# Optimization experiments

Hardware: AMD Instinct MI355X
Metric: run time of the kernel (lower is better)

Reference implementation:

```python
import jax, jax.numpy as jnp
import numpy as np

HEADS = 8
DIM_HEAD = 64
SCALE = DIM_HEAD ** -0.5
POS_DIM = 64


def _sincos_pe(H, W, dim, dtype):
    # matches build_2d_sincos_pos_embed: [1, dim, H, W]
    y = jnp.linspace(-1.0, 1.0, H)[:, None] * jnp.ones((1, W), jnp.float32)
    x = jnp.ones((H, 1), jnp.float32) * jnp.linspace(-1.0, 1.0, W)[None, :]
    omega = 1.0 / (10000.0 ** (jnp.arange(dim // 4, dtype=jnp.float32) / (dim // 4)))
    px = x[..., None] * omega  # [H, W, dim//4]
    py = y[..., None] * omega
    pe = jnp.concatenate([jnp.sin(px), jnp.cos(px), jnp.sin(py), jnp.cos(py)], axis=-1)
    return pe.transpose(2, 0, 1)[None].astype(dtype)


def _conv2d(x, w):
    return jax.lax.conv_general_dilated(
        x, w, (1, 1), 'SAME', dimension_numbers=('NCHW', 'OIHW', 'NCHW'))


def _sobel(d):
    kx = jnp.array([[1, 0, -1], [2, 0, -2], [1, 0, -1]], jnp.float32).reshape(1, 1, 3, 3)
    ky = jnp.array([[1, 2, 1], [0, 0, 0], [-1, -2, -1]], jnp.float32).reshape(1, 1, 3, 3)
    return _conv2d(d, kx), _conv2d(d, ky)


def setup_inputs() -> dict:
    key = jax.random.key(0)
    ks = jax.random.split(key, 8)
    B, C, H, W = 2, 256, 64, 64
    hid = HEADS * DIM_HEAD  # 512
    s = 0.02
    return {
        'x': jax.random.normal(ks[0], (B, C, H, W), jnp.float32),
        'dsm': jax.random.uniform(ks[1], (B, 1, H, W), jnp.float32),
        'wq': jax.random.normal(ks[2], (hid, C), jnp.float32) * s,
        'wkv': jax.random.normal(ks[3], (2 * hid, C + 1), jnp.float32) * s,
        'wout': jax.random.normal(ks[4], (C, hid), jnp.float32) * s,
        'bout': jnp.zeros((C,), jnp.float32),
        'w_hape': jax.random.normal(ks[5], (hid, POS_DIM + 3), jnp.float32) * s,
        'b_hape': jnp.zeros((hid,), jnp.float32),
        'w_alpha': jax.random.normal(ks[6], (1, 1, 3, 3), jnp.float32) * 0.1,
        'b_alpha': jnp.zeros((1,), jnp.float32),
    }


def reference(x, dsm, wq, wkv, wout, bout, w_hape, b_hape, w_alpha, b_alpha):
    B, C, H, W = x.shape
    hid = wq.shape[0]
    # per-sample min-max normalize DSM over spatial dims
    dmin = dsm.min(axis=(2, 3), keepdims=True)
    dmax = dsm.max(axis=(2, 3), keepdims=True)
    d = (dsm - dmin) / (dmax - dmin + 1e-6)
    # HAPE: [PE | h | grad_h] -> 1x1 conv to hidden
    pe = jnp.broadcast_to(_sincos_pe(H, W, POS_DIM, x.dtype), (B, POS_DIM, H, W))
    gx, gy = _sobel(d)
    hape_in = jnp.concatenate([pe, d, gx, gy], axis=1)  # [B, 67, H, W]
    hape_k = jnp.einsum('oc,bchw->bohw', w_hape, hape_in) + b_hape[None, :, None, None]
    # QKV via 1x1 convs
    q = jnp.einsum('oc,bchw->bohw', wq, x)
    kv = jnp.einsum('oc,bchw->bohw', wkv, jnp.concatenate([x, d], axis=1))
    k = kv[:, :hid] + hape_k
    v = kv[:, hid:]
    to_heads = lambda t: t.reshape(B, HEADS, DIM_HEAD, H * W)  # b (h c) x y -> b h c (xy)
    qh = to_heads(q) * SCALE
    kh = to_heads(k)
    vh = to_heads(v)
    sim = jnp.einsum('bhdi,bhdj->bhij', qh, kh)  # [B, h, N, N]
    attn = jax.nn.softmax(sim, axis=-1)
    out = jnp.einsum('bhij,bhdj->bhid', attn, vh)  # [B, h, N, d]
    # b h (x y) d -> b (h d) x y
    out = out.transpose(0, 1, 3, 2).reshape(B, HEADS * DIM_HEAD, H, W)
    out = jnp.einsum('oc,bchw->bohw', wout, out) + bout[None, :, None, None]
    # fine: gradient-magnitude alpha gating
    mag = jnp.sqrt(jnp.maximum(gx, 0.0) ** 2 + jnp.maximum(gy, 0.0) ** 2 + 1e-12)
    alpha = jax.nn.sigmoid(_conv2d(mag, w_alpha) + b_alpha[None, :, None, None])
    return x + out * alpha
```

## Files before the change

kernel.cpp:

```cpp
#include <hip/hip_runtime.h>
#include <math.h>

#define NPOS 4096
#define MTOT 8192
#define KP   352
#define HT 64
#define WT 64
#define NSPLIT 2
#define KEYS_PER (NPOS / NSPLIT)
#define NCH (KEYS_PER / 64)


typedef unsigned short ushortT;
typedef short v8s __attribute__((ext_vector_type(8)));
typedef float v4f __attribute__((ext_vector_type(4)));
typedef unsigned uint2v __attribute__((ext_vector_type(2)));

static __device__ __forceinline__ ushortT bfr(float f) {
    union { float f; unsigned u; } v; v.f = f;
    return (ushortT)((v.u + 0x8000u) >> 16);
}
static __device__ __forceinline__ unsigned pack2bf(float a, float b) {
    union { float f; unsigned u; } ua, ub; ua.f = a; ub.f = b;
    return __builtin_amdgcn_perm(ub.u + 0x8000u, ua.u + 0x8000u, 0x07060302u);
}
static __device__ __forceinline__ unsigned pack2bf_t(float a, float b) {
    union { float f; unsigned u; } ua, ub; ua.f = a; ub.f = b;
    return __builtin_amdgcn_perm(ub.u, ua.u, 0x07060302u);
}
static __device__ __forceinline__ float fexp2(float x) {
#if __has_builtin(__builtin_amdgcn_exp2f)
    return __builtin_amdgcn_exp2f(x);
#else
    return exp2f(x);
#endif
}
static __device__ __forceinline__ float bflo(unsigned u) {
    union { unsigned u; float f; } v; v.u = u << 16; return v.f;
}
static __device__ __forceinline__ float bfhi(unsigned u) {
    union { unsigned u; float f; } v; v.u = u & 0xffff0000u; return v.f;
}

__global__ void k_pre(const float* __restrict__ dsm,
                      const float* __restrict__ walpha, const float* __restrict__ balpha,
                      const float* __restrict__ x,
                      const float* __restrict__ wq, const float* __restrict__ wkv,
                      const float* __restrict__ whape, const float* __restrict__ bhape,
                      const float* __restrict__ wout,
                      ushortT* __restrict__ F, float* __restrict__ alpha,
                      ushortT* __restrict__ Wc, float* __restrict__ biasc,
                      ushortT* __restrict__ woutb) {
    __shared__ __align__(16) ushortT Tl[64][72];
    __shared__ float smn[4], smx[4];
    int role = blockIdx.x;
    int t = threadIdx.x;

    if (role < 32) {
        int idx = role * 256 + t;
        int b = idx / NPOS, n = idx % NPOS;
        int hh = n / WT, ww = n % WT;
        const float* dp = dsm + (size_t)b * NPOS;

        float mn = 1e30f, mx = -1e30f;
        for (int i = t; i < NPOS; i += 256) {
            float v = dp[i];
            mn = fminf(mn, v); mx = fmaxf(mx, v);
        }
        for (int off = 32; off; off >>= 1) {
            mn = fminf(mn, __shfl_xor(mn, off, 64));
            mx = fmaxf(mx, __shfl_xor(mx, off, 64));
        }
        int wid = t >> 6;
        if ((t & 63) == 0) { smn[wid] = mn; smx[wid] = mx; }
        __syncthreads();
        float dmin = fminf(fminf(smn[0], smn[1]), fminf(smn[2], smn[3]));
        float dmax = fmaxf(fmaxf(smx[0], smx[1]), fmaxf(smx[2], smx[3]));
        float inv = 1.0f / (dmax - dmin + 1e-6f);

        float dwin[5][5];
        #pragma unroll
        for (int dy = 0; dy < 5; dy++)
            #pragma unroll
            for (int dx = 0; dx < 5; dx++) {
                int y = hh + dy - 2, xx = ww + dx - 2;
                float v = 0.0f;
                if (y >= 0 && y < HT && xx >= 0 && xx < WT) v = (dp[y * WT + xx] - dmin) * inv;
                dwin[dy][dx] = v;
            }

        float gxc = 0.f, gyc = 0.f, conv = 0.f;
        #pragma unroll
        for (int oy = 0; oy < 3; oy++)
            #pragma unroll
            for (int ox = 0; ox < 3; ox++) {
                int qy = hh + oy - 1, qx = ww + ox - 1;
                float m = 0.0f;
                if (qy >= 0 && qy < HT && qx >= 0 && qx < WT) {
                    float gx = dwin[oy][ox] - dwin[oy][ox + 2]
                             + 2.f * dwin[oy + 1][ox] - 2.f * dwin[oy + 1][ox + 2]
                             + dwin[oy + 2][ox] - dwin[oy + 2][ox + 2];
                    float gy = dwin[oy][ox] + 2.f * dwin[oy][ox + 1] + dwin[oy][ox + 2]
                             - dwin[oy + 2][ox] - 2.f * dwin[oy + 2][ox + 1] - dwin[oy + 2][ox + 2];
                    if (oy == 1 && ox == 1) { gxc = gx; gyc = gy; }
                    float rx = fmaxf(gx, 0.f), ry = fmaxf(gy, 0.f);
                    m = sqrtf(rx * rx + ry * ry + 1e-12f);
                }
                conv += walpha[oy * 3 + ox] * m;
            }
        alpha[idx] = 1.f / (1.f + __expf(-(conv + balpha[0])));

        float xc = -1.f + 2.f * (float)ww / 63.f;
        float yc = -1.f + 2.f * (float)hh / 63.f;
        const float l2w = 13.287712379549449f;
        unsigned pe[32];
        #pragma unroll
        for (int i = 0; i < 16; i += 2) {
            float w0 = exp2f(-(float)i * (l2w / 16.f));
            float w1 = exp2f(-(float)(i + 1) * (l2w / 16.f));
            pe[i / 2]      = pack2bf(__sinf(xc * w0), __sinf(xc * w1));
            pe[8 + i / 2]  = pack2bf(__cosf(xc * w0), __cosf(xc * w1));
            pe[16 + i / 2] = pack2bf(__sinf(yc * w0), __sinf(yc * w1));
            pe[24 + i / 2] = pack2bf(__cosf(yc * w0), __cosf(yc * w1));
        }
        ushortT* fb = F + (size_t)idx * KP;
        uint4* dst = (uint4*)(fb + 256);
        #pragma unroll
        for (int q = 0; q < 8; q++) dst[q] = *(uint4*)&pe[q * 4];
        *(unsigned*)(fb + 320) = pack2bf(dwin[2][2], gxc);
        fb[322] = bfr(gyc);
        fb[323] = 0;
        *(unsigned*)(fb + 324) = 0;
        *(unsigned*)(fb + 326) = 0;
        uint4 z4 = {0, 0, 0, 0};
        *(uint4*)(fb + 328) = z4;
        *(uint4*)(fb + 336) = z4;
        *(uint4*)(fb + 344) = z4;
    } else if (role < 544) {
        int bid = role - 32;
        int nt = (bid & 63) * 64;
        int by = bid >> 6;
        int b = by >> 2, ct = (by & 3) * 64;
        #pragma unroll
        for (int rep = 0; rep < 4; rep++) {
            int row = rep * 16 + (t >> 4), c4 = (t & 15) * 4;
            float4 f4 = *(const float4*)&x[((size_t)(b * 256 + ct + row)) * NPOS + nt + c4];
            Tl[c4 + 0][row] = bfr(f4.x);
            Tl[c4 + 1][row] = bfr(f4.y);
            Tl[c4 + 2][row] = bfr(f4.z);
            Tl[c4 + 3][row] = bfr(f4.w);
        }
        __syncthreads();
        #pragma unroll
        for (int rep = 0; rep < 2; rep++) {
            int slot = rep * 256 + t, row = slot >> 3, c8 = slot & 7;
            *(uint4*)&F[((size_t)(b * 4096 + nt + row)) * KP + ct + c8 * 8] = *(uint4*)&Tl[row][c8 * 8];
        }
    } else {
        int bid = role - 544;
        int idx = bid * 256 + t;
        if (bid < 512) woutb[idx] = bfr(wout[idx]);
        int o = idx / KP, k = idx % KP;
        float v = 0.f;
        if (o < 512) {
            if (k < 256) v = wq[o * 256 + k] * 0.18033688011112042f;
            if (k == 0) biasc[o] = 0.f;
        } else if (o < 1024) {
            int r = o - 512;
            if (k < 256) v = wkv[r * 257 + k];
            else if (k < 320) v = whape[r * 67 + (k - 256)];
            else if (k == 320) v = wkv[r * 257 + 256] + whape[r * 67 + 64];
            else if (k == 321) v = whape[r * 67 + 65];
            else if (k == 322) v = whape[r * 67 + 66];
            if (k == 0) biasc[o] = bhape[r];
        } else {
            int r = o - 512;
            if (k < 256) v = wkv[r * 257 + k];
            else if (k == 320) v = wkv[r * 257 + 256];
            if (k == 0) biasc[o] = 0.f;
        }
        Wc[idx] = bfr(v);
    }
}

__global__ __launch_bounds__(256) void k_gemm1(const ushortT* __restrict__ Wc, const ushortT* __restrict__ F,
                                               const float* __restrict__ biasc,
                                               ushortT* __restrict__ qT, ushortT* __restrict__ kT,
                                               ushortT* __restrict__ vv) {
    __shared__ __align__(16) char smem[256 * 72 * 2];
    ushortT (*Al)[40] = (ushortT(*)[40])smem;
    ushortT (*Bl)[40] = (ushortT(*)[40])(smem + 20480);
    ushortT (*Vt)[72] = (ushortT(*)[72])smem;

    int mt = blockIdx.x * 64;
    int ot = blockIdx.y * 256;
    int t = threadIdx.x, w = t >> 6, lane = t & 63, u = lane & 15, quad = lane >> 4;
    int r4 = t >> 2, ch = t & 3;

    const ushortT* pA0 = Wc + (size_t)(ot +   0 + r4) * KP + ch * 8;
    const ushortT* pA1 = Wc + (size_t)(ot +  64 + r4) * KP + ch * 8;
    const ushortT* pA2 = Wc + (size_t)(ot + 128 + r4) * KP + ch * 8;
    const ushortT* pA3 = Wc + (size_t)(ot + 192 + r4) * KP + ch * 8;
    const ushortT* pB  = F  + (size_t)(mt + r4) * KP + ch * 8;
    uint4 ra0 = *(const uint4*)pA0;
    uint4 ra1 = *(const uint4*)pA1;
    uint4 ra2 = *(const uint4*)pA2;
    uint4 ra3 = *(const uint4*)pA3;
    uint4 rb  = *(const uint4*)pB;

    v4f acc[4][4] = {};
    for (int k0 = 0; k0 < KP; k0 += 32) {
        *(uint4*)&Al[  0 + r4][ch * 8] = ra0;
        *(uint4*)&Al[ 64 + r4][ch * 8] = ra1;
        *(uint4*)&Al[128 + r4][ch * 8] = ra2;
        *(uint4*)&Al[192 + r4][ch * 8] = ra3;
        *(uint4*)&Bl[r4][ch * 8] = rb;
        __syncthreads();
        if (k0 + 32 < KP) {
            pA0 += 32; pA1 += 32; pA2 += 32; pA3 += 32; pB += 32;
            ra0 = *(const uint4*)pA0;
            ra1 = *(const uint4*)pA1;
            ra2 = *(const uint4*)pA2;
            ra3 = *(const uint4*)pA3;
            rb  = *(const uint4*)pB;
        }
        v8s a[4], bb[4];
        #pragma unroll
        for (int rr = 0; rr < 4; rr++) a[rr] = *(v8s*)&Al[w * 64 + rr * 16 + u][quad * 8];
        #pragma unroll
        for (int n4 = 0; n4 < 4; n4++) bb[n4] = *(v8s*)&Bl[n4 * 16 + u][quad * 8];
        #pragma unroll
        for (int rr = 0; rr < 4; rr++)
            #pragma unroll
            for (int n4 = 0; n4 < 4; n4++)
                acc[rr][n4] = __builtin_amdgcn_mfma_f32_16x16x32_bf16(a[rr], bb[n4], acc[rr][n4], 0, 0, 0);
        __syncthreads();
    }
    float bo[4][4];
    #pragma unroll
    for (int rr = 0; rr < 4; rr++)
        #pragma unroll
        for (int r = 0; r < 4; r++) bo[rr][r] = biasc[ot + w * 64 + rr * 16 + quad * 4 + r];
    if (ot < 1024) {
        ushortT* dst = (ot < 512) ? qT : kT;
        #pragma unroll
        for (int rr = 0; rr < 4; rr++) {
            int oo = ot + w * 64 + rr * 16;
            int h = (oo >> 6) & 7;
            int dcol = (oo & 63) + quad * 4;
            #pragma unroll
            for (int n4 = 0; n4 < 4; n4++) {
                int m = mt + n4 * 16 + u;
                uint2 val;
                val.x = pack2bf(acc[rr][n4][0] + bo[rr][0], acc[rr][n4][1] + bo[rr][1]);
                val.y = pack2bf(acc[rr][n4][2] + bo[rr][2], acc[rr][n4][3] + bo[rr][3]);
                *(uint2*)&dst[((size_t)h * MTOT + m) * 64 + dcol] = val;
            }
        }
    } else {
        #pragma unroll
        for (int rr = 0; rr < 4; rr++)
            #pragma unroll
            for (int n4 = 0; n4 < 4; n4++) {
                int ml = n4 * 16 + u;
                #pragma unroll
                for (int r = 0; r < 4; r++)
                    Vt[w * 64 + rr * 16 + quad * 4 + r][ml] = bfr(acc[rr][n4][r] + bo[rr][r]);
            }
        __syncthreads();
        #pragma unroll
        for (int rep = 0; rep < 8; rep++) {
            int slot = rep * 256 + t, row = slot >> 3, c8 = slot & 7;
            *(uint4*)&vv[(size_t)(ot - 1024 + row) * MTOT + mt + c8 * 8] = *(uint4*)&Vt[row][c8 * 8];
        }
    }
}

#define LIDX(row, cb) (((row) << 6) + ((((cb) ^ ((row) & 7))) << 3))
__global__ __launch_bounds__(256, 4) void k_flash(const ushortT* __restrict__ qT,
                                                  const ushortT* __restrict__ kT,
                                                  const ushortT* __restrict__ vv,
                                                  ushortT* __restrict__ Opart,
                                                  float* __restrict__ liPart) {
    __shared__ __align__(16) ushortT Kbuf[2][64 * 64];
    __shared__ __align__(16) ushortT Vbuf[2][64 * 64];

    int it = blockIdx.x;
    int bh = blockIdx.y;
    int half = blockIdx.z;
    int b = bh >> 3, h = bh & 7;
    int colbase = b * NPOS;
    int t = threadIdx.x, w = t >> 6, lane = t & 63, u = lane & 15, quad = lane >> 4;
    int qb = it * 128 + w * 32;

    const ushortT* Qg = qT + ((size_t)h * MTOT + colbase + qb) * 64;
    const ushortT* Kg = kT + ((size_t)h * MTOT + colbase + half * KEYS_PER) * 64;
    const ushortT* Vg = vv + ((size_t)(h * 64)) * MTOT + colbase + half * KEYS_PER;

    int row0 = t >> 3, c80 = t & 7;
    int row1 = 32 + row0;

    unsigned boff[4][2];
    #pragma unroll
    for (int i4 = 0; i4 < 4; i4++) {
        boff[i4][0] = 2u * (unsigned)LIDX(i4 * 16 + u, quad);
        boff[i4][1] = 2u * (unsigned)LIDX(i4 * 16 + u, 4 + quad);
        asm volatile("" : "+v"(boff[i4][0]), "+v"(boff[i4][1]));
    }
    unsigned woff0 = 2u * (unsigned)LIDX(row0, c80);
    unsigned woff1 = 2u * (unsigned)LIDX(row1, c80);
    asm volatile("" : "+v"(woff0), "+v"(woff1));

    v8s bq[2][2];
    #pragma unroll
    for (int g = 0; g < 2; g++)
        #pragma unroll
        for (int hf = 0; hf < 2; hf++)
            bq[g][hf] = *(const v8s*)&Qg[(size_t)(g * 16 + u) * 64 + hf * 32 + quad * 8];

    v8s ones;
    #pragma unroll
    for (int i = 0; i < 8; i++) ones[i] = (short)0x3F80;

    v4f li4[2] = {};
    v4f O[4][2] = {};

    uint4 kr0 = *(const uint4*)&Kg[(size_t)row0 * 64 + c80 * 8];
    uint4 kr1 = *(const uint4*)&Kg[(size_t)row1 * 64 + c80 * 8];
    uint4 vr0 = *(const uint4*)&Vg[(size_t)row0 * MTOT + c80 * 8];
    uint4 vr1 = *(const uint4*)&Vg[(size_t)row1 * MTOT + c80 * 8];

    #pragma unroll 2
    for (int jc = 0; jc < NCH; jc++) {
        int cur = jc & 1;
        char* KbW = (char*)&Kbuf[cur][0];
        char* VbW = (char*)&Vbuf[cur][0];
        *(uint4*)(KbW + woff0) = kr0;
        *(uint4*)(KbW + woff1) = kr1;
        *(uint4*)(VbW + woff0) = vr0;
        *(uint4*)(VbW + woff1) = vr1;
        __syncthreads();
        if (jc + 1 < NCH) {
            int jb = (jc + 1) * 64;
            kr0 = *(const uint4*)&Kg[(size_t)(jb + row0) * 64 + c80 * 8];
            kr1 = *(const uint4*)&Kg[(size_t)(jb + row1) * 64 + c80 * 8];
            vr0 = *(const uint4*)&Vg[(size_t)row0 * MTOT + jb + c80 * 8];
            vr1 = *(const uint4*)&Vg[(size_t)row1 * MTOT + jb + c80 * 8];
        }

        const char* Kb = (const char*)&Kbuf[cur][0];
        const char* Vb = (const char*)&Vbuf[cur][0];

        v8s bp[2][2];
        #pragma unroll
        for (int kp = 0; kp < 2; kp++) {
            unsigned pk0[2][2], pk1[2][2];
            #pragma unroll
            for (int kk = 0; kk < 2; kk++) {
                int k4 = kp * 2 + kk;
                v8s ak0 = *(const v8s*)(Kb + boff[k4][0]);
                v8s ak1 = *(const v8s*)(Kb + boff[k4][1]);
                v4f st[2];
                __builtin_amdgcn_s_setprio(1);
                #pragma unroll
                for (int g = 0; g < 2; g++) {
                    st[g] = (v4f){0.f, 0.f, 0.f, 0.f};
                    st[g] = __builtin_amdgcn_mfma_f32_16x16x32_bf16(ak0, bq[g][0], st[g], 0, 0, 0);
                    st[g] = __builtin_amdgcn_mfma_f32_16x16x32_bf16(ak1, bq[g][1], st[g], 0, 0, 0);
                }
                __builtin_amdgcn_s_setprio(0);
                #pragma unroll
                for (int g = 0; g < 2; g++) {
                    float p0 = fexp2(st[g][0]);
                    float p1 = fexp2(st[g][1]);
                    float p2 = fexp2(st[g][2]);
                    float p3 = fexp2(st[g][3]);
                    pk0[g][kk] = pack2bf_t(p0, p1);
                    pk1[g][kk] = pack2bf_t(p2, p3);
                }
            }
            #pragma unroll
            for (int g = 0; g < 2; g++) {
                uint2v r0s = __builtin_amdgcn_permlane32_swap(pk0[g][0], pk0[g][1], false, false);
                uint2v r1s = __builtin_amdgcn_permlane32_swap(pk1[g][0], pk1[g][1], false, false);
                uint2v t0 = __builtin_amdgcn_permlane16_swap(r0s.x, r0s.y, false, false);
                uint2v t1 = __builtin_amdgcn_permlane16_swap(r1s.x, r1s.y, false, false);
                union { uint4 u4; v8s s; } cv;
                cv.u4.x = t0.x; cv.u4.y = t1.x; cv.u4.z = t0.y; cv.u4.w = t1.y;
                bp[g][kp] = cv.s;
            }
        }

        __builtin_amdgcn_s_setprio(1);
        #pragma unroll
        for (int g = 0; g < 2; g++) {
            li4[g] = __builtin_amdgcn_mfma_f32_16x16x32_bf16(ones, bp[g][0], li4[g], 0, 0, 0);
            li4[g] = __builtin_amdgcn_mfma_f32_16x16x32_bf16(ones, bp[g][1], li4[g], 0, 0, 0);
        }
        #pragma unroll
        for (int d4 = 0; d4 < 4; d4++) {
            v8s av0 = *(const v8s*)(Vb + boff[d4][0]);
            v8s av1 = *(const v8s*)(Vb + boff[d4][1]);
            #pragma unroll
            for (int g = 0; g < 2; g++) {
                O[d4][g] = __builtin_amdgcn_mfma_f32_16x16x32_bf16(av0, bp[g][0], O[d4][g], 0, 0, 0);
                O[d4][g] = __builtin_amdgcn_mfma_f32_16x16x32_bf16(av1, bp[g][1], O[d4][g], 0, 0, 0);
            }
        }
        __builtin_amdgcn_s_setprio(0);
    }

    #pragma unroll
    for (int g = 0; g < 2; g++) {
        int q = qb + g * 16 + u;
        size_t m2 = (size_t)(half * 2 + b) * 4096 + q;
        size_t base = m2 * 512 + h * 64;
        #pragma unroll
        for (int d4 = 0; d4 < 4; d4++) {
            uint2 o2;
            o2.x = pack2bf(O[d4][g][0], O[d4][g][1]);
            o2.y = pack2bf(O[d4][g][2], O[d4][g][3]);
            *(uint2*)&Opart[base + d4 * 16 + quad * 4] = o2;
        }
        if (quad == 0) liPart[m2 * 8 + h] = li4[g][0];
    }
}

__global__ __launch_bounds__(256) void k_gemm2(const ushortT* __restrict__ woutb,
                                               const ushortT* __restrict__ Opart,
                                               const float* __restrict__ liPart,
                                               const float* __restrict__ bout, const float* __restrict__ x,
                                               const float* __restrict__ alpha, float* __restrict__ out) {
    __shared__ __align__(16) ushortT Al[128][40];
    __shared__ __align__(16) ushortT Bl[64][40];
    int mt = blockIdx.x * 64;
    int ot = blockIdx.y * 128;
    int t = threadIdx.x, w = t >> 6, lane = t & 63, u = lane & 15, quad = lane >> 4;
    int r4 = t >> 2, ch = t & 3;
    int m = mt + r4;

    float linv[8];
    #pragma unroll
    for (int h = 0; h < 8; h++)
        linv[h] = 1.f / (liPart[(size_t)m * 8 + h] + liPart[(size_t)(8192 + m) * 8 + h]);

    const ushortT* pA0 = woutb + (size_t)(ot + r4) * 512 + ch * 8;
    const ushortT* pA1 = woutb + (size_t)(ot + 64 + r4) * 512 + ch * 8;
    const ushortT* pO0 = Opart + (size_t)m * 512 + ch * 8;
    const ushortT* pO1 = Opart + (size_t)(8192 + m) * 512 + ch * 8;
    uint4 ra0 = *(const uint4*)pA0;
    uint4 ra1 = *(const uint4*)pA1;
    uint4 ro0 = *(const uint4*)pO0;
    uint4 ro1 = *(const uint4*)pO1;

    v4f acc[2][4] = {};
    for (int k0 = 0; k0 < 512; k0 += 32) {
        int h = (k0 + ch * 8) >> 6;
        float iv = linv[h];
        uint4 bv;
        bv.x = pack2bf((bflo(ro0.x) + bflo(ro1.x)) * iv, (bfhi(ro0.x) + bfhi(ro1.x)) * iv);
        bv.y = pack2bf((bflo(ro0.y) + bflo(ro1.y)) * iv, (bfhi(ro0.y) + bfhi(ro1.y)) * iv);
        bv.z = pack2bf((bflo(ro0.z) + bflo(ro1.z)) * iv, (bfhi(ro0.z) + bfhi(ro1.z)) * iv);
        bv.w = pack2bf((bflo(ro0.w) + bflo(ro1.w)) * iv, (bfhi(ro0.w) + bfhi(ro1.w)) * iv);
        *(uint4*)&Al[r4][ch * 8] = ra0;
        *(uint4*)&Al[64 + r4][ch * 8] = ra1;
        *(uint4*)&Bl[r4][ch * 8] = bv;
        __syncthreads();
        if (k0 + 32 < 512) {
            pA0 += 32; pA1 += 32; pO0 += 32; pO1 += 32;
            ra0 = *(const uint4*)pA0;
            ra1 = *(const uint4*)pA1;
            ro0 = *(const uint4*)pO0;
            ro1 = *(const uint4*)pO1;
        }
        v8s a[2], bb[4];
        #pragma unroll
        for (int rr = 0; rr < 2; rr++) a[rr] = *(v8s*)&Al[w * 32 + rr * 16 + u][quad * 8];
        #pragma unroll
        for (int n4 = 0; n4 < 4; n4++) bb[n4] = *(v8s*)&Bl[n4 * 16 + u][quad * 8];
        #pragma unroll
        for (int rr = 0; rr < 2; rr++)
            #pragma unroll
            for (int n4 = 0; n4 < 4; n4++)
                acc[rr][n4] = __builtin_amdgcn_mfma_f32_16x16x32_bf16(a[rr], bb[n4], acc[rr][n4], 0, 0, 0);
        __syncthreads();
    }
    int b = mt >> 12, n0 = mt & 4095;
    #pragma unroll
    for (int rr = 0; rr < 2; rr++) {
        int obase = ot + w * 32 + rr * 16 + quad * 4;
        float bo[4];
        #pragma unroll
        for (int r = 0; r < 4; r++) bo[r] = bout[obase + r];
        #pragma unroll
        for (int n4 = 0; n4 < 4; n4++) {
            int n = n0 + n4 * 16 + u;
            float al = alpha[(size_t)b * NPOS + n];
            #pragma unroll
            for (int r = 0; r < 4; r++) {
                size_t xi = ((size_t)(b * 256 + obase + r)) * NPOS + n;
                out[xi] = x[xi] + (acc[rr][n4][r] + bo[r]) * al;
            }
        }
    }
}

extern "C" void kernel_launch(void* const* d_in, const int* in_sizes, int n_in,
                              void* d_out, int out_size, void* d_ws, size_t ws_size,
                              hipStream_t stream) {
    const float* x      = (const float*)d_in[0];
    const float* dsm    = (const float*)d_in[1];
    const float* wq     = (const float*)d_in[2];
    const float* wkv    = (const float*)d_in[3];
    const float* wout   = (const float*)d_in[4];
    const float* bout   = (const float*)d_in[5];
    const float* whape  = (const float*)d_in[6];
    const float* bhape  = (const float*)d_in[7];
    const float* walpha = (const float*)d_in[8];
    const float* balpha = (const float*)d_in[9];
    float* out = (float*)d_out;
    float* ws  = (float*)d_ws;

    size_t off = 0;
    float* alpha = ws + off; off += (size_t)2 * NPOS;
    float* biasc = ws + off; off += 2048;
    float* liPart = ws + off; off += (size_t)NSPLIT * MTOT * 8;
    ushortT* Opart = (ushortT*)(ws + off); off += (size_t)NSPLIT * MTOT * 512 / 2;
    ushortT* F     = (ushortT*)(ws + off); off += (size_t)MTOT * KP / 2;
    ushortT* Wc    = (ushortT*)(ws + off); off += (size_t)1536 * KP / 2;
    ushortT* woutb = (ushortT*)(ws + off); off += (size_t)256 * 512 / 2;
    ushortT* qT    = (ushortT*)(ws + off); off += (size_t)8 * MTOT * 64 / 2;
    ushortT* kT    = (ushortT*)(ws + off); off += (size_t)8 * MTOT * 64 / 2;
    ushortT* vv    = (ushortT*)(ws + off); off += (size_t)512 * MTOT / 2;
    (void)in_sizes; (void)n_in; (void)out_size; (void)ws_size;

    k_pre<<<2656, 256, 0, stream>>>(dsm, walpha, balpha, x, wq, wkv, whape, bhape, wout,
                                    F, alpha, Wc, biasc, woutb);
    k_gemm1<<<dim3(128, 6), 256, 0, stream>>>(Wc, F, biasc, qT, kT, vv);
    k_flash<<<dim3(32, 16, NSPLIT), 256, 0, stream>>>(qT, kT, vv, Opart, liPart);
    k_gemm2<<<dim3(128, 2), 256, 0, stream>>>(woutb, Opart, liPart, bout, x, alpha, out);
}
```

Measured before the change: 198.4 us.

## Remap block indices per XCD and halve gemm2 column tile

```diff
diff --git a/kernel.cpp b/kernel.cpp
--- a/kernel.cpp
+++ b/kernel.cpp
@@ -192,8 +192,14 @@
     ushortT (*Bl)[40] = (ushortT(*)[40])(smem + 20480);
     ushortT (*Vt)[72] = (ushortT(*)[72])smem;
 
-    int mt = blockIdx.x * 64;
-    int ot = blockIdx.y * 256;
+    int fid = blockIdx.x;
+    int xcd = fid & 7;
+    int rr_ = fid >> 3;
+    int yt = rr_ % 6;
+    int xt = xcd + 8 * (rr_ / 6);
+    int mt = xt * 64;
+    int ot = yt * 256;
+
     int t = threadIdx.x, w = t >> 6, lane = t & 63, u = lane & 15, quad = lane >> 4;
     int r4 = t >> 2, ch = t & 3;
 
@@ -285,9 +291,15 @@
     __shared__ __align__(16) ushortT Kbuf[2][64 * 64];
     __shared__ __align__(16) ushortT Vbuf[2][64 * 64];
 
-    int it = blockIdx.x;
-    int bh = blockIdx.y;
-    int half = blockIdx.z;
+    int fid = blockIdx.x;
+    int xcd = fid & 7;
+    int rr_ = fid >> 3;
+    int it = rr_ & 31;
+    int chi = rr_ >> 5;
+    int c = xcd + 8 * chi;
+    int bh = c & 15;
+    int half = c >> 4;
+
     int b = bh >> 3, h = bh & 7;
     int colbase = b * NPOS;
     int t = threadIdx.x, w = t >> 6, lane = t & 63, u = lane & 15, quad = lane >> 4;
@@ -432,57 +444,65 @@
                                                const float* __restrict__ bout, const float* __restrict__ x,
                                                const float* __restrict__ alpha, float* __restrict__ out) {
     __shared__ __align__(16) ushortT Al[128][40];
-    __shared__ __align__(16) ushortT Bl[64][40];
-    int mt = blockIdx.x * 64;
+    __shared__ __align__(16) ushortT Bl[32][40];
+    int mt = blockIdx.x * 32;
     int ot = blockIdx.y * 128;
     int t = threadIdx.x, w = t >> 6, lane = t & 63, u = lane & 15, quad = lane >> 4;
     int r4 = t >> 2, ch = t & 3;
-    int m = mt + r4;
-
-    float linv[8];
-    #pragma unroll
-    for (int h = 0; h < 8; h++)
-        linv[h] = 1.f / (liPart[(size_t)m * 8 + h] + liPart[(size_t)(8192 + m) * 8 + h]);
 
     const ushortT* pA0 = woutb + (size_t)(ot + r4) * 512 + ch * 8;
     const ushortT* pA1 = woutb + (size_t)(ot + 64 + r4) * 512 + ch * 8;
-    const ushortT* pO0 = Opart + (size_t)m * 512 + ch * 8;
-    const ushortT* pO1 = Opart + (size_t)(8192 + m) * 512 + ch * 8;
     uint4 ra0 = *(const uint4*)pA0;
     uint4 ra1 = *(const uint4*)pA1;
-    uint4 ro0 = *(const uint4*)pO0;
-    uint4 ro1 = *(const uint4*)pO1;
-
-    v4f acc[2][4] = {};
+
+    const ushortT* pO0 = 0; const ushortT* pO1 = 0;
+    uint4 ro0 = {}, ro1 = {};
+    float linv[8];
+    int bm = mt + r4;
+    if (t < 128) {
+        #pragma unroll
+        for (int h = 0; h < 8; h++)
+            linv[h] = 1.f / (liPart[(size_t)bm * 8 + h] + liPart[(size_t)(8192 + bm) * 8 + h]);
+        pO0 = Opart + (size_t)bm * 512 + ch * 8;
+        pO1 = Opart + (size_t)(8192 + bm) * 512 + ch * 8;
+        ro0 = *(const uint4*)pO0;
+        ro1 = *(const uint4*)pO1;
+    }
+
+    v4f acc[2][2] = {};
     for (int k0 = 0; k0 < 512; k0 += 32) {
-        int h = (k0 + ch * 8) >> 6;
-        float iv = linv[h];
-        uint4 bv;
-        bv.x = pack2bf((bflo(ro0.x) + bflo(ro1.x)) * iv, (bfhi(ro0.x) + bfhi(ro1.x)) * iv);
-        bv.y = pack2bf((bflo(ro0.y) + bflo(ro1.y)) * iv, (bfhi(ro0.y) + bfhi(ro1.y)) * iv);
-        bv.z = pack2bf((bflo(ro0.z) + bflo(ro1.z)) * iv, (bfhi(ro0.z) + bfhi(ro1.z)) * iv);
-        bv.w = pack2bf((bflo(ro0.w) + bflo(ro1.w)) * iv, (bfhi(ro0.w) + bfhi(ro1.w)) * iv);
         *(uint4*)&Al[r4][ch * 8] = ra0;
         *(uint4*)&Al[64 + r4][ch * 8] = ra1;
-        *(uint4*)&Bl[r4][ch * 8] = bv;
+        if (t < 128) {
+            int h = (k0 + ch * 8) >> 6;
+            float iv = linv[h];
+            uint4 bv;
+            bv.x = pack2bf((bflo(ro0.x) + bflo(ro1.x)) * iv, (bfhi(ro0.x) + bfhi(ro1.x)) * iv);
+            bv.y = pack2bf((bflo(ro0.y) + bflo(ro1.y)) * iv, (bfhi(ro0.y) + bfhi(ro1.y)) * iv);
+            bv.z = pack2bf((bflo(ro0.z) + bflo(ro1.z)) * iv, (bfhi(ro0.z) + bfhi(ro1.z)) * iv);
+            bv.w = pack2bf((bflo(ro0.w) + bflo(ro1.w)) * iv, (bfhi(ro0.w) + bfhi(ro1.w)) * iv);
+            *(uint4*)&Bl[r4][ch * 8] = bv;
+        }
         __syncthreads();
         if (k0 + 32 < 512) {
-            pA0 += 32; pA1 += 32; pO0 += 32; pO1 += 32;
+            pA0 += 32; pA1 += 32;
             ra0 = *(const uint4*)pA0;
             ra1 = *(const uint4*)pA1;
-            ro0 = *(const uint4*)pO0;
-            ro1 = *(const uint4*)pO1;
-        }
-        v8s a[2], bb[4];
-        #pragma unroll
-        for (int rr = 0; rr < 2; rr++) a[rr] = *(v8s*)&Al[w * 32 + rr * 16 + u][quad * 8];
-        #pragma unroll
-        for (int n4 = 0; n4 < 4; n4++) bb[n4] = *(v8s*)&Bl[n4 * 16 + u][quad * 8];
-        #pragma unroll
-        for (int rr = 0; rr < 2; rr++)
-            #pragma unroll
-            for (int n4 = 0; n4 < 4; n4++)
-                acc[rr][n4] = __builtin_amdgcn_mfma_f32_16x16x32_bf16(a[rr], bb[n4], acc[rr][n4], 0, 0, 0);
+            if (t < 128) {
+                pO0 += 32; pO1 += 32;
+                ro0 = *(const uint4*)pO0;
+                ro1 = *(const uint4*)pO1;
+            }
+        }
+        v8s a[2], bb[2];
+        a[0] = *(v8s*)&Al[w * 32 + u][quad * 8];
+        a[1] = *(v8s*)&Al[w * 32 + 16 + u][quad * 8];
+        bb[0] = *(v8s*)&Bl[u][quad * 8];
+        bb[1] = *(v8s*)&Bl[16 + u][quad * 8];
+        acc[0][0] = __builtin_amdgcn_mfma_f32_16x16x32_bf16(a[0], bb[0], acc[0][0], 0, 0, 0);
+        acc[0][1] = __builtin_amdgcn_mfma_f32_16x16x32_bf16(a[0], bb[1], acc[0][1], 0, 0, 0);
+        acc[1][0] = __builtin_amdgcn_mfma_f32_16x16x32_bf16(a[1], bb[0], acc[1][0], 0, 0, 0);
+        acc[1][1] = __builtin_amdgcn_mfma_f32_16x16x32_bf16(a[1], bb[1], acc[1][1], 0, 0, 0);
         __syncthreads();
     }
     int b = mt >> 12, n0 = mt & 4095;
@@ -493,7 +513,7 @@
         #pragma unroll
         for (int r = 0; r < 4; r++) bo[r] = bout[obase + r];
         #pragma unroll
-        for (int n4 = 0; n4 < 4; n4++) {
+        for (int n4 = 0; n4 < 2; n4++) {
             int n = n0 + n4 * 16 + u;
             float al = alpha[(size_t)b * NPOS + n];
             #pragma unroll
@@ -536,7 +556,7 @@
 
     k_pre<<<2656, 256, 0, stream>>>(dsm, walpha, balpha, x, wq, wkv, whape, bhape, wout,
                                     F, alpha, Wc, biasc, woutb);
-    k_gemm1<<<dim3(128, 6), 256, 0, stream>>>(Wc, F, biasc, qT, kT, vv);
-    k_flash<<<dim3(32, 16, NSPLIT), 256, 0, stream>>>(qT, kT, vv, Opart, liPart);
-    k_gemm2<<<dim3(128, 2), 256, 0, stream>>>(woutb, Opart, liPart, bout, x, alpha, out);
-}
+    k_gemm1<<<768, 256, 0, stream>>>(Wc, F, biasc, qT, kT, vv);
+    k_flash<<<1024, 256, 0, stream>>>(qT, kT, vv, Opart, liPart);
+    k_gemm2<<<dim3(256, 2), 256, 0, stream>>>(woutb, Opart, liPart, bout, x, alpha, out);
+}
```

New measurement: 197.9 us (median of 2 runs). Within noise of the previous version (-0.2%).
